# Performance work log

Measured on AMD Instinct MI355X. Metric: run time of the kernel, lower is better.

The kernel has to match this reference:

```python
import jax, jax.numpy as jnp
import numpy as np

HEADS = 16

def setup_inputs() -> dict:
    key = jax.random.key(0)
    k1, k2, k3 = jax.random.split(key, 3)
    B, N, C = 4, 4096, 1024
    x = jax.random.normal(k1, (B, N, C), dtype=jnp.float32)
    w_qkv = jax.random.normal(k2, (3 * C, C), dtype=jnp.float32) * (C ** -0.5)
    w_proj = jax.random.normal(k3, (C, C), dtype=jnp.float32) * (C ** -0.5)
    b_proj = jnp.zeros((C,), dtype=jnp.float32)
    return {"x": x, "w_qkv": w_qkv, "w_proj": w_proj, "b_proj": b_proj}

def reference(x, w_qkv, w_proj, b_proj):
    B, N, C = x.shape
    H = HEADS
    D = C // H
    qkv = x @ w_qkv.T                      # [B,N,3C]
    q, k, v = jnp.split(qkv, 3, axis=-1)   # each [B,N,C]
    # b n (h d) -> b h d n
    def to_bhdn(t):
        return t.reshape(B, N, H, D).transpose(0, 2, 3, 1)
    q = jax.nn.relu(to_bhdn(q))
    k = jax.nn.relu(to_bhdn(k))
    v = to_bhdn(v)
    eps = jnp.finfo(q.dtype).eps
    ksum = k.sum(axis=-1)                                   # [B,H,D]
    z = 1.0 / (jnp.einsum('bhd,bhdn->bhn', ksum, q) + eps)  # [B,H,N]
    context = jnp.einsum('bhdn,bhen->bhde', v, k)            # v @ k^T, [B,H,D,D]
    out = jnp.einsum('bhde,bhen->bhdn', context, q)          # [B,H,D,N]
    out = out * z[:, :, None, :]
    # b h d n -> b n (h d)
    out = out.transpose(0, 3, 1, 2).reshape(B, N, C)
    return out @ w_proj.T + b_proj
```

## Files before the change

kernel.cpp:

```cpp
#include <hip/hip_runtime.h>
#include <hip/hip_bf16.h>


typedef __bf16 bf16;
typedef __bf16 bf16x8 __attribute__((ext_vector_type(8)));
typedef __bf16 bf16x4 __attribute__((ext_vector_type(4)));
typedef float  f32x4  __attribute__((ext_vector_type(4)));

#define MFMA16(a, b, c) __builtin_amdgcn_mfma_f32_16x16x32_bf16((a), (b), (c), 0, 0, 0)

__device__ __forceinline__ void gload_lds16(const bf16* g, bf16* l) {
  __builtin_amdgcn_global_load_lds(
      (const __attribute__((address_space(1))) void*)g,
      (__attribute__((address_space(3))) void*)l, 16, 0, 0);
}

__global__ __launch_bounds__(256) void cvt3(const float* __restrict__ x,  bf16* __restrict__ xb,
                                            const float* __restrict__ wq, bf16* __restrict__ wqb,
                                            const float* __restrict__ wp, bf16* __restrict__ wpb) {
  const long stride = (long)gridDim.x * 256;
  for (long i4 = (long)blockIdx.x * 256 + threadIdx.x; i4 < 5242880; i4 += stride) {
    const float* s; bf16* d; long off;
    if (i4 < 4194304)      { s = x;  d = xb;  off = i4; }
    else if (i4 < 4980736) { s = wq; d = wqb; off = i4 - 4194304; }
    else                   { s = wp; d = wpb; off = i4 - 4980736; }
    const float4 v = *(const float4*)(s + off * 4);
    bf16x4 o;
    o[0] = (bf16)v.x; o[1] = (bf16)v.y; o[2] = (bf16)v.z; o[3] = (bf16)v.w;
    *(bf16x4*)(d + off * 4) = o;
  }
}

template <int LDC, typename CO>
__global__ __launch_bounds__(256) void gemm_bt(const bf16* __restrict__ A,
                                               const bf16* __restrict__ Bm,
                                               CO* __restrict__ Co,
                                               const float* __restrict__ bias,
                                               const int reluRows) {
  __shared__ bf16 As[128 * 32];
  __shared__ bf16 Bs[128 * 32];
  const int tid  = threadIdx.x;
  const int lane = tid & 63;
  const int w    = tid >> 6;
  const int wr   = w >> 1;
  const int wc   = w & 1;

  const int gx = gridDim.x, gy = gridDim.y;
  const int nwg = gx * gy;
  const int id  = blockIdx.x + gx * blockIdx.y;
  const int sid = (nwg & 7) ? id : ((id & 7) * (nwg >> 3) + (id >> 3));
  const int j0 = (sid % gx) * 128;
  const int i0 = (sid / gx) * 128;

  const int srow = lane >> 2;
  const int scol = (lane & 3) * 8;
  const bf16* Ag = A  + (long)(i0 + w * 32 + srow) * 1024 + scol;
  const bf16* Bg = Bm + (long)(j0 + w * 32 + srow) * 1024 + scol;
  bf16* Asw = As + w * 32 * 32;
  bf16* Bsw = Bs + w * 32 * 32;

  const int r15  = lane & 15;
  const int koff = (lane >> 4) * 8;

  f32x4 acc[4][4] = {};

  for (int kk = 0; kk < 1024; kk += 32) {
    gload_lds16(Ag + kk,             Asw);
    gload_lds16(Ag + kk + 16 * 1024, Asw + 16 * 32);
    gload_lds16(Bg + kk,             Bsw);
    gload_lds16(Bg + kk + 16 * 1024, Bsw + 16 * 32);
    __syncthreads();
    bf16x8 af[4], bfm[4];
#pragma unroll
    for (int t = 0; t < 4; ++t)
      af[t] = *(const bf16x8*)(As + (wr * 64 + t * 16 + r15) * 32 + koff);
#pragma unroll
    for (int u = 0; u < 4; ++u)
      bfm[u] = *(const bf16x8*)(Bs + (wc * 64 + u * 16 + r15) * 32 + koff);
#pragma unroll
    for (int t = 0; t < 4; ++t)
#pragma unroll
      for (int u = 0; u < 4; ++u)
        acc[t][u] = MFMA16(af[t], bfm[u], acc[t][u]);
    __syncthreads();
  }

  const bool doRelu = (i0 < reluRows);
  const int rbase = i0 + wr * 64;
  const int cbase = j0 + wc * 64;
#pragma unroll
  for (int t = 0; t < 4; ++t) {
    const int r0 = rbase + t * 16 + (lane >> 4) * 4;
#pragma unroll
    for (int u = 0; u < 4; ++u) {
      const int cc = cbase + u * 16 + r15;
      const float bv = bias ? bias[cc] : 0.0f;
#pragma unroll
      for (int jj = 0; jj < 4; ++jj) {
        float v = acc[t][u][jj] + bv;
        if (doRelu) v = fmaxf(v, 0.0f);
        Co[(long)(r0 + jj) * LDC + cc] = (CO)v;
      }
    }
  }
}

template <int LDC, typename CO>
__global__ __launch_bounds__(512, 2) void gemm256(const bf16* __restrict__ A,
                                                  const bf16* __restrict__ Bm,
                                                  CO* __restrict__ Co,
                                                  const float* __restrict__ bias,
                                                  const int reluRows) {
  __shared__ bf16 As[2][256 * 64];
  __shared__ bf16 Bs[2][256 * 64];
  const int tid  = threadIdx.x;
  const int lane = tid & 63;
  const int w    = tid >> 6;
  const int wm   = w >> 2;
  const int wn   = w & 3;

  const int gx = gridDim.x, gy = gridDim.y;
  const int nwg = gx * gy;
  const int id  = blockIdx.x + gx * blockIdx.y;
  const int sid = (id & 7) * (nwg >> 3) + (id >> 3);
  int bx, by;
  if (gx < gy) { bx = sid % gx; by = sid / gx; }
  else         { by = sid % gy; bx = sid / gy; }
  const int i0 = by * 256;
  const int j0 = bx * 256;

  const int lr = lane >> 3;
  const int lc = (lane & 7) ^ lr;
  const bf16* Agl = A  + (long)(i0 + 8 * w + lr) * 1024 + lc * 8;
  const bf16* Bgl = Bm + (long)(j0 + 8 * w + lr) * 1024 + lc * 8;
  const int wofs = w * 512;

  const int r15 = lane & 15, g = lane >> 4;
  const int ck[2] = { ((0 + g) ^ (r15 & 7)) * 8, ((4 + g) ^ (r15 & 7)) * 8 };
  const int arow = (wm * 128 + r15) * 64;
  const int brow = (wn * 64 + r15) * 64;

  f32x4 acc[8][4] = {};

#pragma unroll
  for (int q = 0; q < 4; ++q) {
    gload_lds16(Agl + q * 65536, &As[0][q * 4096 + wofs]);
    gload_lds16(Bgl + q * 65536, &Bs[0][q * 4096 + wofs]);
  }

  for (int kt = 0; kt < 16; ++kt) {
    const int cur = kt & 1;
    if (kt < 15) {
      const long ko = (long)(kt + 1) * 64;
#pragma unroll
      for (int q = 0; q < 4; ++q) {
        gload_lds16(Agl + ko + q * 65536, &As[cur ^ 1][q * 4096 + wofs]);
        gload_lds16(Bgl + ko + q * 65536, &Bs[cur ^ 1][q * 4096 + wofs]);
      }
      asm volatile("s_waitcnt vmcnt(8)" ::: "memory");
    } else {
      asm volatile("s_waitcnt vmcnt(0)" ::: "memory");
    }
    __builtin_amdgcn_s_barrier();
    __builtin_amdgcn_sched_barrier(0);

    const bf16* Ab = &As[cur][arow];
    const bf16* Bb = &Bs[cur][brow];
#pragma unroll
    for (int ks = 0; ks < 2; ++ks) {
      bf16x8 af[8], bfr[4];
#pragma unroll
      for (int fm = 0; fm < 8; ++fm)
        af[fm] = *(const bf16x8*)(Ab + fm * 1024 + ck[ks]);
#pragma unroll
      for (int fn = 0; fn < 4; ++fn)
        bfr[fn] = *(const bf16x8*)(Bb + fn * 1024 + ck[ks]);
      __builtin_amdgcn_s_setprio(1);
#pragma unroll
      for (int fm = 0; fm < 8; ++fm)
#pragma unroll
        for (int fn = 0; fn < 4; ++fn)
          acc[fm][fn] = MFMA16(af[fm], bfr[fn], acc[fm][fn]);
      __builtin_amdgcn_s_setprio(0);
    }
    asm volatile("s_waitcnt lgkmcnt(0)" ::: "memory");
    __builtin_amdgcn_sched_barrier(0);
    __builtin_amdgcn_s_barrier();
  }

  const bool doRelu = (i0 < reluRows);
#pragma unroll
  for (int fm = 0; fm < 8; ++fm) {
    const int r0 = i0 + wm * 128 + fm * 16 + g * 4;
#pragma unroll
    for (int fn = 0; fn < 4; ++fn) {
      const int cc = j0 + wn * 64 + fn * 16 + r15;
      const float bv = bias ? bias[cc] : 0.0f;
#pragma unroll
      for (int jj = 0; jj < 4; ++jj) {
        float v = acc[fm][fn][jj] + bv;
        if (doRelu) v = fmaxf(v, 0.0f);
        Co[(long)(r0 + jj) * LDC + cc] = (CO)v;
      }
    }
  }
}

__global__ __launch_bounds__(256) void ctx_kernel(const bf16* __restrict__ QKV,
                                                  float* __restrict__ ctx_part,
                                                  float* __restrict__ ksum_part) {
  const int bh = blockIdx.x;
  const int s  = blockIdx.y;
  const int b  = bh >> 4, h = bh & 15;
  const int tid = threadIdx.x, lane = tid & 63, w = tid >> 6;
  const long ldq = 16384;
  const bf16* Kp = QKV + (long)(1024 + h * 64) * ldq + b * 4096 + s * 512;
  const bf16* Vp = QKV + (long)(2048 + h * 64) * ldq + b * 4096 + s * 512;

  const int r15  = lane & 15;
  const int koff = (lane >> 4) * 8;

  f32x4 acc[4] = {};
#pragma unroll 4
  for (int n = 0; n < 512; n += 32) {
    const bf16x8 a = *(const bf16x8*)(Vp + (long)(w * 16 + r15) * ldq + n + koff);
#pragma unroll
    for (int u = 0; u < 4; ++u) {
      const bf16x8 kb = *(const bf16x8*)(Kp + (long)(u * 16 + r15) * ldq + n + koff);
      acc[u] = MFMA16(a, kb, acc[u]);
    }
  }
  float* cp = ctx_part + (long)(bh * 8 + s) * 4096;
#pragma unroll
  for (int u = 0; u < 4; ++u)
#pragma unroll
    for (int jj = 0; jj < 4; ++jj) {
      const int d = w * 16 + (lane >> 4) * 4 + jj;
      const int e = u * 16 + r15;
      cp[d * 64 + e] = acc[u][jj];
    }

  const int e = tid >> 2, q4 = tid & 3;
  const bf16* kr = Kp + (long)e * ldq + q4 * 128;
  float sum = 0.0f;
#pragma unroll
  for (int i = 0; i < 128; i += 8) {
    const bf16x8 v = *(const bf16x8*)(kr + i);
#pragma unroll
    for (int jj = 0; jj < 8; ++jj) sum += (float)v[jj];
  }
  sum += __shfl_xor(sum, 1);
  sum += __shfl_xor(sum, 2);
  if (q4 == 0) ksum_part[(bh * 8 + s) * 64 + e] = sum;
}

__global__ __launch_bounds__(256) void out_kernel(const bf16* __restrict__ QKV,
                                                  const float* __restrict__ ctx_part,
                                                  const float* __restrict__ ksum_part,
                                                  bf16* __restrict__ O) {
  __shared__ bf16 ctx_lds[64 * 88];
  __shared__ bf16 qlds[256 * 80];
  __shared__ float ksum_lds[64];
  __shared__ float zlds[256];

  const int nc = blockIdx.x;
  const int bh = blockIdx.y;
  const int b = bh >> 4, h = bh & 15;
  const int tid = threadIdx.x, lane = tid & 63, w = tid >> 6;
  const int n0 = nc * 256;
  const long ldq = 16384;

  const float* cp = ctx_part + (long)bh * 8 * 4096;
#pragma unroll
  for (int r = 0; r < 16; ++r) {
    const int idx = tid + r * 256;
    float v = 0.0f;
#pragma unroll
    for (int s2 = 0; s2 < 8; ++s2) v += cp[s2 * 4096 + idx];
    ctx_lds[(idx >> 6) * 88 + (idx & 63)] = (bf16)v;
  }
  if (tid < 64) {
    float v = 0.0f;
#pragma unroll
    for (int s2 = 0; s2 < 8; ++s2) v += ksum_part[(bh * 8 + s2) * 64 + tid];
    ksum_lds[tid] = v;
  }
  {
    const bf16* Qp = QKV + (long)(h * 64) * ldq + b * 4096 + n0;
    const int e = tid >> 2, seg = tid & 3;
    const bf16* qr = Qp + (long)e * ldq + seg * 64;
#pragma unroll
    for (int i = 0; i < 64; i += 8) {
      const bf16x8 v = *(const bf16x8*)(qr + i);
#pragma unroll
      for (int jj = 0; jj < 8; ++jj) qlds[(seg * 64 + i + jj) * 80 + e] = v[jj];
    }
  }
  __syncthreads();

  {
    float a = 0.0f;
    const bf16* qrow = qlds + tid * 80;
#pragma unroll
    for (int d = 0; d < 64; ++d) a += (float)qrow[d] * ksum_lds[d];
    zlds[tid] = 1.0f / (a + 1.1920929e-07f);
  }
  const int r15 = lane & 15;
  const int koff = (lane >> 4) * 8;
  bf16x8 afr[4][2];
#pragma unroll
  for (int t = 0; t < 4; ++t)
#pragma unroll
    for (int s2 = 0; s2 < 2; ++s2)
      afr[t][s2] = *(const bf16x8*)(ctx_lds + (t * 16 + r15) * 88 + s2 * 32 + koff);
  __syncthreads();

#pragma unroll
  for (int nt = 0; nt < 4; ++nt) {
    const int ntile = w * 4 + nt;
    bf16x8 bfr[2];
#pragma unroll
    for (int s2 = 0; s2 < 2; ++s2)
      bfr[s2] = *(const bf16x8*)(qlds + (ntile * 16 + r15) * 80 + s2 * 32 + koff);
    f32x4 accn[4] = {};
#pragma unroll
    for (int t = 0; t < 4; ++t) {
      accn[t] = MFMA16(afr[t][0], bfr[0], accn[t]);
      accn[t] = MFMA16(afr[t][1], bfr[1], accn[t]);
    }
    const int ncol = n0 + ntile * 16 + r15;
    const float zv = zlds[ntile * 16 + r15];
    bf16* orow = O + (long)(b * 4096 + ncol) * 1024 + h * 64;
#pragma unroll
    for (int t = 0; t < 4; ++t) {
      const int d0 = t * 16 + (lane >> 4) * 4;
      bf16x4 pk;
#pragma unroll
      for (int jj = 0; jj < 4; ++jj) pk[jj] = (bf16)(accn[t][jj] * zv);
      *(bf16x4*)(orow + d0) = pk;
    }
  }
}

extern "C" void kernel_launch(void* const* d_in, const int* in_sizes, int n_in,
                              void* d_out, int out_size, void* d_ws, size_t ws_size,
                              hipStream_t stream) {
  const float* x      = (const float*)d_in[0];
  const float* w_qkv  = (const float*)d_in[1];
  const float* w_proj = (const float*)d_in[2];
  const float* b_proj = (const float*)d_in[3];
  float* out = (float*)d_out;

  char* ws = (char*)d_ws;
  bf16*  QKV       = (bf16*)ws;
  float* ctx_part  = (float*)(ws + 100663296);
  float* ksum_part = (float*)(ws + 100663296 + 8388608);
  bf16*  xb        = (bf16*)(ws + 109182976);
  bf16*  O         = xb;
  bf16*  wqkvb     = (bf16*)(ws + 109182976 + 33554432);
  bf16*  wprojb    = (bf16*)(ws + 109182976 + 33554432 + 6291456);

  cvt3<<<2048, 256, 0, stream>>>(x, xb, w_qkv, wqkvb, w_proj, wprojb);
  gemm_bt<16384, bf16><<<dim3(128, 24), 256, 0, stream>>>(wqkvb, xb, QKV, nullptr, 2048);
  ctx_kernel<<<dim3(64, 8), 256, 0, stream>>>(QKV, ctx_part, ksum_part);
  out_kernel<<<dim3(16, 64), 256, 0, stream>>>(QKV, ctx_part, ksum_part, O);
  gemm256<1024, float><<<dim3(4, 64), 512, 0, stream>>>(O, wprojb, out, b_proj, 0);
}
```

Baseline: 266.6 us.

## Double K-step to 64 in QKV GEMM with XOR-swizzled LDS layout

The QKV projection GEMM now stages 64-wide K slices per iteration instead of 32, which halves the number of barrier pairs and doubles the MFMAs issued per synchronisation. LDS rows are XOR-swizzled in 16-byte chunks to avoid bank conflicts on the wider rows. The grouped workgroup ID remapping for L2 locality is dropped in favour of plain blockIdx ordering. LDS use per block doubles to 32 KB, which may reduce occupancy, and losing the remap may hurt cache reuse.

After: 254.7 us. 4.5% less time.

```diff
diff --git a/kernel.cpp b/kernel.cpp
--- a/kernel.cpp
+++ b/kernel.cpp
@@ -32,56 +32,58 @@
 }
 
 template <int LDC, typename CO>
-__global__ __launch_bounds__(256) void gemm_bt(const bf16* __restrict__ A,
-                                               const bf16* __restrict__ Bm,
-                                               CO* __restrict__ Co,
-                                               const float* __restrict__ bias,
-                                               const int reluRows) {
-  __shared__ bf16 As[128 * 32];
-  __shared__ bf16 Bs[128 * 32];
+__global__ __launch_bounds__(256) void gemm_bt64(const bf16* __restrict__ A,
+                                                 const bf16* __restrict__ Bm,
+                                                 CO* __restrict__ Co,
+                                                 const float* __restrict__ bias,
+                                                 const int reluRows) {
+  __shared__ bf16 As[128 * 64];
+  __shared__ bf16 Bs[128 * 64];
   const int tid  = threadIdx.x;
   const int lane = tid & 63;
   const int w    = tid >> 6;
   const int wr   = w >> 1;
   const int wc   = w & 1;
-
-  const int gx = gridDim.x, gy = gridDim.y;
-  const int nwg = gx * gy;
-  const int id  = blockIdx.x + gx * blockIdx.y;
-  const int sid = (nwg & 7) ? id : ((id & 7) * (nwg >> 3) + (id >> 3));
-  const int j0 = (sid % gx) * 128;
-  const int i0 = (sid / gx) * 128;
-
-  const int srow = lane >> 2;
-  const int scol = (lane & 3) * 8;
-  const bf16* Ag = A  + (long)(i0 + w * 32 + srow) * 1024 + scol;
-  const bf16* Bg = Bm + (long)(j0 + w * 32 + srow) * 1024 + scol;
-  bf16* Asw = As + w * 32 * 32;
-  bf16* Bsw = Bs + w * 32 * 32;
-
-  const int r15  = lane & 15;
-  const int koff = (lane >> 4) * 8;
+  const int j0 = blockIdx.x * 128;
+  const int i0 = blockIdx.y * 128;
+
+  const int lr8 = lane >> 3;
+  const int lc  = (lane & 7) ^ lr8;
+  const bf16* Ag = A  + (long)(i0 + w * 32 + lr8) * 1024 + lc * 8;
+  const bf16* Bg = Bm + (long)(j0 + w * 32 + lr8) * 1024 + lc * 8;
+  bf16* Asw = As + w * 32 * 64;
+  bf16* Bsw = Bs + w * 32 * 64;
+
+  const int r15 = lane & 15, g = lane >> 4;
+  const int ac0 = ((0 + g) ^ (r15 & 7)) * 8;
+  const int ac1 = ((4 + g) ^ (r15 & 7)) * 8;
 
   f32x4 acc[4][4] = {};
 
-  for (int kk = 0; kk < 1024; kk += 32) {
-    gload_lds16(Ag + kk,             Asw);
-    gload_lds16(Ag + kk + 16 * 1024, Asw + 16 * 32);
-    gload_lds16(Bg + kk,             Bsw);
-    gload_lds16(Bg + kk + 16 * 1024, Bsw + 16 * 32);
+  for (int kk = 0; kk < 1024; kk += 64) {
+#pragma unroll
+    for (int q = 0; q < 4; ++q) {
+      gload_lds16(Ag + kk + q * 8 * 1024, Asw + q * 512);
+      gload_lds16(Bg + kk + q * 8 * 1024, Bsw + q * 512);
+    }
     __syncthreads();
-    bf16x8 af[4], bfm[4];
-#pragma unroll
-    for (int t = 0; t < 4; ++t)
-      af[t] = *(const bf16x8*)(As + (wr * 64 + t * 16 + r15) * 32 + koff);
-#pragma unroll
-    for (int u = 0; u < 4; ++u)
-      bfm[u] = *(const bf16x8*)(Bs + (wc * 64 + u * 16 + r15) * 32 + koff);
-#pragma unroll
-    for (int t = 0; t < 4; ++t)
-#pragma unroll
-      for (int u = 0; u < 4; ++u)
-        acc[t][u] = MFMA16(af[t], bfm[u], acc[t][u]);
+    bf16x8 af[4][2], bfm[4][2];
+#pragma unroll
+    for (int t = 0; t < 4; ++t) {
+      const int ra = (wr * 64 + t * 16 + r15) * 64;
+      af[t][0] = *(const bf16x8*)(As + ra + ac0);
+      af[t][1] = *(const bf16x8*)(As + ra + ac1);
+      const int rb = (wc * 64 + t * 16 + r15) * 64;
+      bfm[t][0] = *(const bf16x8*)(Bs + rb + ac0);
+      bfm[t][1] = *(const bf16x8*)(Bs + rb + ac1);
+    }
+#pragma unroll
+    for (int ks = 0; ks < 2; ++ks)
+#pragma unroll
+      for (int t = 0; t < 4; ++t)
+#pragma unroll
+        for (int u = 0; u < 4; ++u)
+          acc[t][u] = MFMA16(af[t][ks], bfm[u][ks], acc[t][u]);
     __syncthreads();
   }
 
@@ -90,7 +92,7 @@
   const int cbase = j0 + wc * 64;
 #pragma unroll
   for (int t = 0; t < 4; ++t) {
-    const int r0 = rbase + t * 16 + (lane >> 4) * 4;
+    const int r0 = rbase + t * 16 + g * 4;
 #pragma unroll
     for (int u = 0; u < 4; ++u) {
       const int cc = cbase + u * 16 + r15;
@@ -361,7 +363,7 @@
   bf16*  wprojb    = (bf16*)(ws + 109182976 + 33554432 + 6291456);
 
   cvt3<<<2048, 256, 0, stream>>>(x, xb, w_qkv, wqkvb, w_proj, wprojb);
-  gemm_bt<16384, bf16><<<dim3(128, 24), 256, 0, stream>>>(wqkvb, xb, QKV, nullptr, 2048);
+  gemm_bt64<16384, bf16><<<dim3(128, 24), 256, 0, stream>>>(wqkvb, xb, QKV, nullptr, 2048);
   ctx_kernel<<<dim3(64, 8), 256, 0, stream>>>(QKV, ctx_part, ksum_part);
   out_kernel<<<dim3(16, 64), 256, 0, stream>>>(QKV, ctx_part, ksum_part, O);
   gemm256<1024, float><<<dim3(4, 64), 512, 0, stream>>>(O, wprojb, out, b_proj, 0);
```
